# Performance work log

Hardware: AMD Instinct MI355X
Metric: run time of the kernel (lower is better)

## Reference

```python
import jax, jax.numpy as jnp
import numpy as np

B, T, D, H = 2, 2048, 1024, 16
DK = D // H  # 64


def setup_inputs() -> dict:
    key = jax.random.key(0)
    ks = jax.random.split(key, 13)
    s = 1.0 / np.sqrt(D)
    return {
        "x": jax.random.normal(ks[0], (B, T, D), jnp.float32),
        "Wq_w": jax.random.normal(ks[1], (D, D), jnp.float32) * s,
        "Wq_b": jax.random.normal(ks[2], (D,), jnp.float32) * 0.01,
        "Wk_w": jax.random.normal(ks[3], (D, D), jnp.float32) * s,
        "Wk_b": jax.random.normal(ks[4], (D,), jnp.float32) * 0.01,
        "Wv_w": jax.random.normal(ks[5], (D, D), jnp.float32) * s,
        "Wv_b": jax.random.normal(ks[6], (D,), jnp.float32) * 0.01,
        "Wo_w": jax.random.normal(ks[7], (D, D), jnp.float32) * s,
        "Wo_b": jax.random.normal(ks[8], (D,), jnp.float32) * 0.01,
        "qr": jax.random.normal(ks[9], (B, H, T, DK), jnp.float32),
        "qi": jax.random.normal(ks[10], (B, H, T, DK), jnp.float32),
        "kr": jax.random.normal(ks[11], (B, H, T, DK), jnp.float32),
        "ki": jax.random.normal(ks[12], (B, H, T, DK), jnp.float32),
    }


def _heads(y):
    # [B,T,D] -> [B,H,T,DK]
    return y.reshape(B, T, H, DK).transpose(0, 2, 1, 3)


def reference(x, Wq_w, Wq_b, Wk_w, Wk_b, Wv_w, Wv_b, Wo_w, Wo_b, qr, qi, kr, ki):
    Q = _heads(x @ Wq_w.T + Wq_b)
    K = _heads(x @ Wk_w.T + Wk_b)
    V = _heads(x @ Wv_w.T + Wv_b)
    # quantum noise: sin(atan2(imag, real))
    Q = Q + jnp.sin(jnp.arctan2(qi, qr))
    K = K + jnp.sin(jnp.arctan2(ki, kr))
    # Recursive fractal attention collapses: branches are identical and
    # deterministic, so (A1+A2)/2 == depth-0 attention at every level.
    scores = jnp.einsum("bhtd,bhsd->bhts", Q, K) / np.sqrt(DK).astype(np.float32)
    weights = jax.nn.softmax(scores, axis=-1)
    attn = jnp.einsum("bhts,bhsd->bhtd", weights, V)  # [B,H,T,DK]
    out = attn.transpose(0, 2, 1, 3).reshape(B, T, D)
    return out @ Wo_w.T + Wo_b
```

## Files before the change

### kernel.cpp

```cpp
#include <hip/hip_runtime.h>
#include <hip/hip_fp16.h>
#include <stdint.h>

typedef _Float16 half_t;
typedef _Float16 hf2 __attribute__((ext_vector_type(2)));
typedef _Float16 hf4 __attribute__((ext_vector_type(4)));
typedef _Float16 hf8 __attribute__((ext_vector_type(8)));
typedef float f32x16 __attribute__((ext_vector_type(16)));
typedef unsigned uint2_t __attribute__((ext_vector_type(2)));

#define LOG2E 1.4426950408889634f
#define SM_M 16.0f

__device__ __forceinline__ void gload16(const void* g, void* l) {
  __builtin_amdgcn_global_load_lds(
      (const __attribute__((address_space(1))) unsigned int*)g,
      (__attribute__((address_space(3))) unsigned int*)l, 16, 0, 0);
}

__device__ __forceinline__ unsigned packrtz(float a, float b) {
  auto h = __builtin_amdgcn_cvt_pkrtz(a, b);
  union { decltype(h) h2; unsigned u; } c;
  c.h2 = h;
  return c.u;
}

__global__ __launch_bounds__(256) void cvt_kernel(
    const float* __restrict__ x, const float* __restrict__ wq,
    const float* __restrict__ wk, const float* __restrict__ wv,
    const float* __restrict__ wo, half_t* __restrict__ xh,
    half_t* __restrict__ wh) {
  long e = ((long)blockIdx.x * 256 + threadIdx.x) * 16;
  const float* src;
  half_t* dst;
  if (e < 4194304L) {
    src = x + e;
    dst = xh + e;
  } else {
    long j = e - 4194304L;
    int w = (int)(j >> 20);
    long off = j & 1048575L;
    src = (w == 0 ? wq : w == 1 ? wk : w == 2 ? wv : wo) + off;
    dst = wh + ((long)w << 20) + off;
  }
  const float4* s4 = (const float4*)src;
  float4 f0 = s4[0], f1 = s4[1], f2 = s4[2], f3 = s4[3];
  hf8 o0 = {(half_t)f0.x, (half_t)f0.y, (half_t)f0.z, (half_t)f0.w,
            (half_t)f1.x, (half_t)f1.y, (half_t)f1.z, (half_t)f1.w};
  hf8 o1 = {(half_t)f2.x, (half_t)f2.y, (half_t)f2.z, (half_t)f2.w,
            (half_t)f3.x, (half_t)f3.y, (half_t)f3.z, (half_t)f3.w};
  *(hf8*)dst = o0;
  *(hf8*)(dst + 8) = o1;
}

__device__ __forceinline__ void gemm_core(const half_t* __restrict__ A,
                                          const half_t* __restrict__ Bt,
                                          int m0, int n0, half_t* ldsA,
                                          half_t* ldsB, f32x16 acc[2][2]) {
  const int tid = threadIdx.x;
  const int wid = tid >> 6;
  const int lane = tid & 63;
  const int l31 = lane & 31;
  const int hh = lane >> 5;
  const int wm = wid >> 1, wn = wid & 1;

#pragma unroll
  for (int mt = 0; mt < 2; mt++)
#pragma unroll
    for (int nt = 0; nt < 2; nt++)
#pragma unroll
      for (int i = 0; i < 16; i++) acc[mt][nt][i] = 0.f;

  for (int kt = 0; kt < 16; ++kt) {
#pragma unroll
    for (int i = 0; i < 4; i++) {
      int c = i * 256 + tid;
      int row = c >> 3;
      int c16 = (c & 7) ^ (row & 7);
      gload16(A + (long)(m0 + row) * 1024 + kt * 64 + c16 * 8,
              ldsA + i * 2048 + wid * 512);
      gload16(Bt + (long)(n0 + row) * 1024 + kt * 64 + c16 * 8,
              ldsB + i * 2048 + wid * 512);
    }
    __syncthreads();
#pragma unroll
    for (int kc = 0; kc < 4; kc++) {
      hf8 af[2], bf[2];
#pragma unroll
      for (int mt = 0; mt < 2; mt++) {
        int row = wm * 64 + mt * 32 + l31;
        af[mt] = *(const hf8*)((const char*)ldsA + row * 128 +
                               ((kc * 32 + hh * 16) ^ ((row & 7) << 4)));
      }
#pragma unroll
      for (int nt = 0; nt < 2; nt++) {
        int row = wn * 64 + nt * 32 + l31;
        bf[nt] = *(const hf8*)((const char*)ldsB + row * 128 +
                               ((kc * 32 + hh * 16) ^ ((row & 7) << 4)));
      }
#pragma unroll
      for (int mt = 0; mt < 2; mt++)
#pragma unroll
        for (int nt = 0; nt < 2; nt++)
          acc[mt][nt] = __builtin_amdgcn_mfma_f32_32x32x16_f16(
              af[mt], bf[nt], acc[mt][nt], 0, 0, 0);
    }
    __syncthreads();
  }
}

__global__ __launch_bounds__(256, 2) void proj_kernel(
    const half_t* __restrict__ xh, const half_t* __restrict__ wh,
    const float* __restrict__ bq, const float* __restrict__ bk,
    const float* __restrict__ bv, const float* __restrict__ qr,
    const float* __restrict__ qi, const float* __restrict__ kr,
    const float* __restrict__ ki, half_t* __restrict__ Qh,
    half_t* __restrict__ Kh, half_t* __restrict__ Vth) {
  __shared__ __align__(16) half_t ldsA[128 * 64];
  __shared__ __align__(16) half_t ldsB[128 * 64];
  const int z = blockIdx.z;
  const half_t* Bt = wh + (size_t)z * 1048576;
  const int m0 = blockIdx.x * 128, n0 = blockIdx.y * 128;
  f32x16 acc[2][2];
  gemm_core(xh, Bt, m0, n0, ldsA, ldsB, acc);

  const int tid = threadIdx.x;
  const int wid = tid >> 6;
  const int lane = tid & 63;
  const int l31 = lane & 31;
  const int hh = lane >> 5;
  const int wm = wid >> 1, wn = wid & 1;
  const float* bias = (z == 0) ? bq : (z == 1) ? bk : bv;
  const float* nr = (z == 0) ? qr : kr;
  const float* ni = (z == 0) ? qi : ki;
  const float scale = (z == 0) ? (0.125f * LOG2E) : 1.0f;

#pragma unroll
  for (int nt = 0; nt < 2; nt++) {
    const int n = n0 + wn * 64 + nt * 32 + l31;
    const float bsv = bias[n];
    const int hd = n >> 6, d = n & 63;
#pragma unroll
    for (int mt = 0; mt < 2; mt++) {
      const int mbase = m0 + wm * 64 + mt * 32;
      if (z == 2) {
#pragma unroll
        for (int g = 0; g < 4; g++) {
          const int m = mbase + 8 * g + 4 * hh;
          const int bb = m >> 11, tt = m & 2047;
          hf4 pk;
#pragma unroll
          for (int i2 = 0; i2 < 4; i2++)
            pk[i2] = (half_t)(acc[mt][nt][4 * g + i2] + bsv);
          *(hf4*)(Vth + (((size_t)(bb * 16 + hd) * 64 + d) * 2048 + tt)) = pk;
        }
      } else {
        half_t* dstp = (z == 0) ? Qh : Kh;
#pragma unroll
        for (int r = 0; r < 16; r++) {
          const int m = mbase + (r & 3) + 8 * (r >> 2) + 4 * hh;
          const int bb = m >> 11, tt = m & 2047;
          const size_t idx = ((size_t)(bb * 16 + hd) * 2048 + tt) * 64 + d;
          float v = acc[mt][nt][r] + bsv;
          const float a_ = nr[idx], b_ = ni[idx];
          v += b_ * rsqrtf(a_ * a_ + b_ * b_);
          dstp[idx] = (half_t)(v * scale);
        }
      }
    }
  }
}

__global__ __launch_bounds__(512, 4) void attn_kernel(
    const half_t* __restrict__ Qh, const half_t* __restrict__ Kh,
    const half_t* __restrict__ Vth, half_t* __restrict__ ah) {
  __shared__ __align__(16) char smem[65536];
  const int tid = threadIdx.x, wid = tid >> 6, lane = tid & 63;
  const int l31 = lane & 31, hh = lane >> 5;
  const int qw = wid & 3, g = wid >> 2;
  const int bh = blockIdx.y;
  const int b = bh >> 4, hd = bh & 15;
  const int t = blockIdx.x * 128 + qw * 32 + l31;

  half_t* Kl = (half_t*)(smem + g * 32768);
  half_t* Vl = Kl + 8192;

  const half_t* qrow = Qh + ((size_t)bh * 2048 + t) * 64;
  hf8 qf[4];
#pragma unroll
  for (int kc = 0; kc < 4; kc++) qf[kc] = *(const hf8*)(qrow + kc * 16 + hh * 8);

  f32x16 ot[2];
#pragma unroll
  for (int dt = 0; dt < 2; dt++)
#pragma unroll
    for (int i = 0; i < 16; i++) ot[dt][i] = 0.f;
  float lrun = 0.f;

  const half_t* Kb = Kh + (size_t)bh * 2048 * 64;
  const half_t* Vb = Vth + (size_t)bh * 64 * 2048;
  const int kvbase = g * 1024;

  {
    const int kv0 = kvbase;
#pragma unroll
    for (int i = 0; i < 2; i++) {
      int c = i * 256 + qw * 64 + lane;
      int row = c >> 3, c16 = (c & 7) ^ (row & 7);
      gload16(Kb + (size_t)(kv0 + row) * 64 + c16 * 8, Kl + i * 2048 + qw * 512);
      gload16(Vb + (size_t)row * 2048 + kv0 + c16 * 8, Vl + i * 2048 + qw * 512);
    }
  }
  __syncthreads();

  for (int tile = 0; tile < 16; ++tile) {
    const int cur = tile & 1;
    if (tile < 15) {
      const int kv0 = kvbase + (tile + 1) * 64;
      half_t* Kd = Kl + (cur ^ 1) * 4096;
      half_t* Vd = Vl + (cur ^ 1) * 4096;
#pragma unroll
      for (int i = 0; i < 2; i++) {
        int c = i * 256 + qw * 64 + lane;
        int row = c >> 3, c16 = (c & 7) ^ (row & 7);
        gload16(Kb + (size_t)(kv0 + row) * 64 + c16 * 8, Kd + i * 2048 + qw * 512);
        gload16(Vb + (size_t)row * 2048 + kv0 + c16 * 8, Vd + i * 2048 + qw * 512);
      }
    }
    const char* Kc = (const char*)(Kl + cur * 4096);
    const char* Vc = (const char*)(Vl + cur * 4096);

    f32x16 s[2];
#pragma unroll
    for (int kt = 0; kt < 2; kt++)
#pragma unroll
      for (int i = 0; i < 16; i++) s[kt][i] = 0.f;
#pragma unroll
    for (int kt = 0; kt < 2; kt++)
#pragma unroll
      for (int kc = 0; kc < 4; kc++) {
        int row = kt * 32 + l31;
        hf8 kf = *(const hf8*)(Kc + row * 128 +
                               ((kc * 32 + hh * 16) ^ ((row & 7) << 4)));
        s[kt] = __builtin_amdgcn_mfma_f32_32x32x16_f16(kf, qf[kc], s[kt], 0, 0, 0);
      }

    float psum = 0.f;
#pragma unroll
    for (int kt = 0; kt < 2; kt++)
#pragma unroll
      for (int r = 0; r < 16; r++) {
        float p = exp2f(s[kt][r] - SM_M);
        s[kt][r] = p;
        psum += p;
      }
    psum += __shfl_xor(psum, 32, 64);
    lrun += psum;

#pragma unroll
    for (int kt = 0; kt < 2; kt++) {
      unsigned pw[8];
#pragma unroll
      for (int j = 0; j < 8; j++) pw[j] = packrtz(s[kt][2 * j], s[kt][2 * j + 1]);
#pragma unroll
      for (int sub = 0; sub < 2; sub++) {
        const int kc = kt * 2 + sub;
        unsigned a0 = pw[sub * 4 + 0], a1 = pw[sub * 4 + 1];
        unsigned a2 = pw[sub * 4 + 2], a3 = pw[sub * 4 + 3];
        union { unsigned u[4]; hf8 v; } pu;
#if __has_builtin(__builtin_amdgcn_permlane32_swap)
        uint2_t r02 = __builtin_amdgcn_permlane32_swap(a0, a2, false, false);
        uint2_t r13 = __builtin_amdgcn_permlane32_swap(a1, a3, false, false);
        pu.u[0] = r02[0];
        pu.u[1] = r13[0];
        pu.u[2] = r02[1];
        pu.u[3] = r13[1];
#else
        unsigned x0 = __shfl_xor(a0, 32, 64), x1 = __shfl_xor(a1, 32, 64);
        unsigned x2 = __shfl_xor(a2, 32, 64), x3 = __shfl_xor(a3, 32, 64);
        pu.u[0] = hh ? x2 : a0;
        pu.u[1] = hh ? x3 : a1;
        pu.u[2] = hh ? a2 : x0;
        pu.u[3] = hh ? a3 : x1;
#endif
#pragma unroll
        for (int dt = 0; dt < 2; dt++) {
          int row = dt * 32 + l31;
          hf8 vf = *(const hf8*)(Vc + row * 128 +
                                 ((kc * 32 + hh * 16) ^ ((row & 7) << 4)));
          ot[dt] = __builtin_amdgcn_mfma_f32_32x32x16_f16(vf, pu.v, ot[dt], 0, 0, 0);
        }
      }
    }
    __syncthreads();
  }

  float* cb = (float*)smem;
  float* lb = (float*)(smem + 32768);
  if (g == 1) {
#pragma unroll
    for (int dt = 0; dt < 2; dt++)
#pragma unroll
      for (int i = 0; i < 16; i++)
        cb[((qw * 2 + dt) * 16 + i) * 64 + lane] = ot[dt][i];
    lb[qw * 64 + lane] = lrun;
  }
  __syncthreads();
  if (g == 0) {
#pragma unroll
    for (int dt = 0; dt < 2; dt++)
#pragma unroll
      for (int i = 0; i < 16; i++)
        ot[dt][i] += cb[((qw * 2 + dt) * 16 + i) * 64 + lane];
    const float inv = 1.0f / (lrun + lb[qw * 64 + lane]);
    const size_t obase = ((size_t)b * 2048 + t) * 1024 + hd * 64;
#pragma unroll
    for (int dt = 0; dt < 2; dt++)
#pragma unroll
      for (int gg = 0; gg < 4; gg++) {
        hf4 pk;
#pragma unroll
        for (int i2 = 0; i2 < 4; i2++)
          pk[i2] = (half_t)(ot[dt][4 * gg + i2] * inv);
        *(hf4*)(ah + obase + dt * 32 + 8 * gg + 4 * hh) = pk;
      }
  }
}

__global__ __launch_bounds__(256, 2) void outproj_kernel(
    const half_t* __restrict__ ah, const half_t* __restrict__ woh,
    const float* __restrict__ bo, float* __restrict__ out) {
  __shared__ __align__(16) half_t ldsA[128 * 64];
  __shared__ __align__(16) half_t ldsB[128 * 64];
  const int m0 = blockIdx.x * 128, n0 = blockIdx.y * 128;
  f32x16 acc[2][2];
  gemm_core(ah, woh, m0, n0, ldsA, ldsB, acc);
  const int tid = threadIdx.x, wid = tid >> 6, lane = tid & 63;
  const int l31 = lane & 31, hh = lane >> 5;
  const int wm = wid >> 1, wn = wid & 1;
#pragma unroll
  for (int nt = 0; nt < 2; nt++) {
    const int n = n0 + wn * 64 + nt * 32 + l31;
    const float bsv = bo[n];
#pragma unroll
    for (int mt = 0; mt < 2; mt++) {
      const int mbase = m0 + wm * 64 + mt * 32;
#pragma unroll
      for (int r = 0; r < 16; r++) {
        const int m = mbase + (r & 3) + 8 * (r >> 2) + 4 * hh;
        out[(size_t)m * 1024 + n] = acc[mt][nt][r] + bsv;
      }
    }
  }
}

extern "C" void kernel_launch(void* const* d_in, const int* in_sizes, int n_in,
                              void* d_out, int out_size, void* d_ws,
                              size_t ws_size, hipStream_t stream) {
  const float* x = (const float*)d_in[0];
  const float* Wq = (const float*)d_in[1];
  const float* bq = (const float*)d_in[2];
  const float* Wk = (const float*)d_in[3];
  const float* bk = (const float*)d_in[4];
  const float* Wv = (const float*)d_in[5];
  const float* bv = (const float*)d_in[6];
  const float* Wo = (const float*)d_in[7];
  const float* bo = (const float*)d_in[8];
  const float* qr = (const float*)d_in[9];
  const float* qi = (const float*)d_in[10];
  const float* kr = (const float*)d_in[11];
  const float* ki = (const float*)d_in[12];
  float* out = (float*)d_out;

  char* ws = (char*)d_ws;
  half_t* xh = (half_t*)(ws);
  half_t* wh = (half_t*)(ws + 8388608);
  half_t* Qh = (half_t*)(ws + 16777216);
  half_t* Kh = (half_t*)(ws + 25165824);
  half_t* Vth = (half_t*)(ws + 33554432);
  half_t* ah = (half_t*)(ws + 41943040);

  cvt_kernel<<<dim3(2048), dim3(256), 0, stream>>>(x, Wq, Wk, Wv, Wo, xh, wh);
  proj_kernel<<<dim3(32, 8, 3), dim3(256), 0, stream>>>(
      xh, wh, bq, bk, bv, qr, qi, kr, ki, Qh, Kh, Vth);
  attn_kernel<<<dim3(16, 32), dim3(512), 0, stream>>>(Qh, Kh, Vth, ah);
  outproj_kernel<<<dim3(32, 8), dim3(256), 0, stream>>>(ah, wh + 3 * 1048576, bo,
                                                        out);
}
```

Baseline: 124.5 us.

## Double-buffer GEMM LDS tiles and streamline attention inner loop

The projection GEMMs switch from a single LDS buffer with load-then-sync each k-step to a two-buffer ping-pong, prefetching the next k-tile while the current one is consumed, which halves the barriers. Global and LDS addresses are precomputed once and advanced by pointer increments. The attention loop is unrolled by two with precomputed LDS pointers and folds the softmax offset into the MFMA accumulator init. It also adds s_setprio around the MFMA blocks and defers the cross-half row-sum shuffle to the end. The cost is doubled LDS per GEMM block (64KB), which may reduce occupancy.

After: 185.9 us. 1.49x slower.

```diff
diff --git a/kernel.cpp b/kernel.cpp
--- a/kernel.cpp
+++ b/kernel.cpp
@@ -3,7 +3,6 @@
 #include <stdint.h>
 
 typedef _Float16 half_t;
-typedef _Float16 hf2 __attribute__((ext_vector_type(2)));
 typedef _Float16 hf4 __attribute__((ext_vector_type(4)));
 typedef _Float16 hf8 __attribute__((ext_vector_type(8)));
 typedef float f32x16 __attribute__((ext_vector_type(16)));
@@ -53,6 +52,40 @@
   *(hf8*)(dst + 8) = o1;
 }
 
+__device__ __forceinline__ void gemm_tile(bool stage, int cur,
+                                          const half_t* const gA[4],
+                                          const half_t* const gB[4],
+                                          half_t* ldsA, half_t* ldsB, int wid,
+                                          const char* const ab[4],
+                                          const char* const bb[4],
+                                          f32x16 acc[2][2]) {
+  if (stage) {
+#pragma unroll
+    for (int i = 0; i < 4; i++) {
+      gload16(gA[i], ldsA + (cur ^ 1) * 8192 + i * 2048 + wid * 512);
+      gload16(gB[i], ldsB + (cur ^ 1) * 8192 + i * 2048 + wid * 512);
+    }
+  }
+  const int cb = cur * 16384;
+#pragma unroll
+  for (int kc = 0; kc < 4; kc++) {
+    hf8 af[2], bf[2];
+#pragma unroll
+    for (int mt = 0; mt < 2; mt++)
+      af[mt] = *(const hf8*)(ab[kc] + cb + mt * 4096);
+#pragma unroll
+    for (int nt = 0; nt < 2; nt++)
+      bf[nt] = *(const hf8*)(bb[kc] + cb + nt * 4096);
+#pragma unroll
+    for (int mt = 0; mt < 2; mt++)
+#pragma unroll
+      for (int nt = 0; nt < 2; nt++)
+        acc[mt][nt] = __builtin_amdgcn_mfma_f32_32x32x16_f16(
+            af[mt], bf[nt], acc[mt][nt], 0, 0, 0);
+  }
+  __syncthreads();
+}
+
 __device__ __forceinline__ void gemm_core(const half_t* __restrict__ A,
                                           const half_t* __restrict__ Bt,
                                           int m0, int n0, half_t* ldsA,
@@ -71,41 +104,40 @@
 #pragma unroll
       for (int i = 0; i < 16; i++) acc[mt][nt][i] = 0.f;
 
-  for (int kt = 0; kt < 16; ++kt) {
-#pragma unroll
-    for (int i = 0; i < 4; i++) {
-      int c = i * 256 + tid;
-      int row = c >> 3;
-      int c16 = (c & 7) ^ (row & 7);
-      gload16(A + (long)(m0 + row) * 1024 + kt * 64 + c16 * 8,
-              ldsA + i * 2048 + wid * 512);
-      gload16(Bt + (long)(n0 + row) * 1024 + kt * 64 + c16 * 8,
-              ldsB + i * 2048 + wid * 512);
-    }
-    __syncthreads();
-#pragma unroll
-    for (int kc = 0; kc < 4; kc++) {
-      hf8 af[2], bf[2];
-#pragma unroll
-      for (int mt = 0; mt < 2; mt++) {
-        int row = wm * 64 + mt * 32 + l31;
-        af[mt] = *(const hf8*)((const char*)ldsA + row * 128 +
-                               ((kc * 32 + hh * 16) ^ ((row & 7) << 4)));
-      }
-#pragma unroll
-      for (int nt = 0; nt < 2; nt++) {
-        int row = wn * 64 + nt * 32 + l31;
-        bf[nt] = *(const hf8*)((const char*)ldsB + row * 128 +
-                               ((kc * 32 + hh * 16) ^ ((row & 7) << 4)));
-      }
-#pragma unroll
-      for (int mt = 0; mt < 2; mt++)
-#pragma unroll
-        for (int nt = 0; nt < 2; nt++)
-          acc[mt][nt] = __builtin_amdgcn_mfma_f32_32x32x16_f16(
-              af[mt], bf[nt], acc[mt][nt], 0, 0, 0);
-    }
-    __syncthreads();
+  const half_t* gA[4];
+  const half_t* gB[4];
+#pragma unroll
+  for (int i = 0; i < 4; i++) {
+    int c = i * 256 + tid;
+    int row = c >> 3;
+    int c16 = (c & 7) ^ (row & 7);
+    gA[i] = A + (long)(m0 + row) * 1024 + c16 * 8;
+    gB[i] = Bt + (long)(n0 + row) * 1024 + c16 * 8;
+  }
+  const char* ab[4];
+  const char* bb[4];
+#pragma unroll
+  for (int kc = 0; kc < 4; kc++) {
+    int swz = (kc * 32 + hh * 16) ^ ((l31 & 7) << 4);
+    ab[kc] = (const char*)ldsA + wm * 8192 + l31 * 128 + swz;
+    bb[kc] = (const char*)ldsB + wn * 8192 + l31 * 128 + swz;
+  }
+#pragma unroll
+  for (int i = 0; i < 4; i++) {
+    gload16(gA[i], ldsA + i * 2048 + wid * 512);
+    gload16(gB[i], ldsB + i * 2048 + wid * 512);
+    gA[i] += 64;
+    gB[i] += 64;
+  }
+  __syncthreads();
+
+  for (int kp = 0; kp < 8; ++kp) {
+    gemm_tile(true, 0, gA, gB, ldsA, ldsB, wid, ab, bb, acc);
+#pragma unroll
+    for (int i = 0; i < 4; i++) { gA[i] += 64; gB[i] += 64; }
+    gemm_tile(kp < 7, 1, gA, gB, ldsA, ldsB, wid, ab, bb, acc);
+#pragma unroll
+    for (int i = 0; i < 4; i++) { gA[i] += 64; gB[i] += 64; }
   }
 }
 
@@ -116,8 +148,8 @@
     const float* __restrict__ qi, const float* __restrict__ kr,
     const float* __restrict__ ki, half_t* __restrict__ Qh,
     half_t* __restrict__ Kh, half_t* __restrict__ Vth) {
-  __shared__ __align__(16) half_t ldsA[128 * 64];
-  __shared__ __align__(16) half_t ldsB[128 * 64];
+  __shared__ __align__(16) half_t ldsA[2 * 8192];
+  __shared__ __align__(16) half_t ldsB[2 * 8192];
   const int z = blockIdx.z;
   const half_t* Bt = wh + (size_t)z * 1048576;
   const int m0 = blockIdx.x * 128, n0 = blockIdx.y * 128;
@@ -171,6 +203,80 @@
   }
 }
 
+__device__ __forceinline__ void attn_tile(
+    bool stage, int cur, const half_t* gk0, const half_t* gk1,
+    const half_t* gv0, const half_t* gv1, half_t* KV, int qw,
+    const char* const kb[4], const hf8 qf[4], const f32x16& mneg,
+    f32x16 ot[2], float& psAcc) {
+  if (stage) {
+    half_t* Kd = KV + (cur ^ 1) * 4096;
+    gload16(gk0, Kd + qw * 512);
+    gload16(gk1, Kd + 2048 + qw * 512);
+    half_t* Vd = KV + 8192 + (cur ^ 1) * 4096;
+    gload16(gv0, Vd + qw * 512);
+    gload16(gv1, Vd + 2048 + qw * 512);
+  }
+  const int cb = cur * 8192;
+  f32x16 s[2];
+  __builtin_amdgcn_s_setprio(1);
+#pragma unroll
+  for (int kt = 0; kt < 2; kt++) {
+    s[kt] = __builtin_amdgcn_mfma_f32_32x32x16_f16(
+        *(const hf8*)(kb[0] + cb + kt * 4096), qf[0], mneg, 0, 0, 0);
+#pragma unroll
+    for (int kc = 1; kc < 4; kc++)
+      s[kt] = __builtin_amdgcn_mfma_f32_32x32x16_f16(
+          *(const hf8*)(kb[kc] + cb + kt * 4096), qf[kc], s[kt], 0, 0, 0);
+  }
+  __builtin_amdgcn_s_setprio(0);
+
+#pragma unroll
+  for (int kt = 0; kt < 2; kt++) {
+    unsigned pw[8];
+    float pa = 0.f, pb = 0.f;
+#pragma unroll
+    for (int j = 0; j < 8; j++) {
+      float p0 = exp2f(s[kt][2 * j]);
+      float p1 = exp2f(s[kt][2 * j + 1]);
+      pa += p0;
+      pb += p1;
+      pw[j] = packrtz(p0, p1);
+    }
+    psAcc += pa + pb;
+#pragma unroll
+    for (int sub = 0; sub < 2; sub++) {
+      const int kc = kt * 2 + sub;
+      unsigned a0 = pw[sub * 4 + 0], a1 = pw[sub * 4 + 1];
+      unsigned a2 = pw[sub * 4 + 2], a3 = pw[sub * 4 + 3];
+      union { unsigned u[4]; hf8 v; } pu;
+#if __has_builtin(__builtin_amdgcn_permlane32_swap)
+      uint2_t r02 = __builtin_amdgcn_permlane32_swap(a0, a2, false, false);
+      uint2_t r13 = __builtin_amdgcn_permlane32_swap(a1, a3, false, false);
+      pu.u[0] = r02[0];
+      pu.u[1] = r13[0];
+      pu.u[2] = r02[1];
+      pu.u[3] = r13[1];
+#else
+      const int hh_ = (threadIdx.x & 63) >> 5;
+      unsigned x0 = __shfl_xor(a0, 32, 64), x1 = __shfl_xor(a1, 32, 64);
+      unsigned x2 = __shfl_xor(a2, 32, 64), x3 = __shfl_xor(a3, 32, 64);
+      pu.u[0] = hh_ ? x2 : a0;
+      pu.u[1] = hh_ ? x3 : a1;
+      pu.u[2] = hh_ ? a2 : x0;
+      pu.u[3] = hh_ ? a3 : x1;
+#endif
+      __builtin_amdgcn_s_setprio(1);
+#pragma unroll
+      for (int dt = 0; dt < 2; dt++) {
+        hf8 vf = *(const hf8*)(kb[kc] + 16384 + cb + dt * 4096);
+        ot[dt] = __builtin_amdgcn_mfma_f32_32x32x16_f16(vf, pu.v, ot[dt], 0, 0, 0);
+      }
+      __builtin_amdgcn_s_setprio(0);
+    }
+  }
+  __syncthreads();
+}
+
 __global__ __launch_bounds__(512, 4) void attn_kernel(
     const half_t* __restrict__ Qh, const half_t* __restrict__ Kh,
     const half_t* __restrict__ Vth, half_t* __restrict__ ah) {
@@ -182,8 +288,7 @@
   const int b = bh >> 4, hd = bh & 15;
   const int t = blockIdx.x * 128 + qw * 32 + l31;
 
-  half_t* Kl = (half_t*)(smem + g * 32768);
-  half_t* Vl = Kl + 8192;
+  half_t* KV = (half_t*)(smem + g * 32768);
 
   const half_t* qrow = Qh + ((size_t)bh * 2048 + t) * 64;
   hf8 qf[4];
@@ -195,105 +300,50 @@
   for (int dt = 0; dt < 2; dt++)
 #pragma unroll
     for (int i = 0; i < 16; i++) ot[dt][i] = 0.f;
-  float lrun = 0.f;
+  f32x16 mneg;
+#pragma unroll
+  for (int i = 0; i < 16; i++) mneg[i] = -SM_M;
+  float psAcc = 0.f;
 
   const half_t* Kb = Kh + (size_t)bh * 2048 * 64;
   const half_t* Vb = Vth + (size_t)bh * 64 * 2048;
   const int kvbase = g * 1024;
 
-  {
-    const int kv0 = kvbase;
-#pragma unroll
-    for (int i = 0; i < 2; i++) {
-      int c = i * 256 + qw * 64 + lane;
-      int row = c >> 3, c16 = (c & 7) ^ (row & 7);
-      gload16(Kb + (size_t)(kv0 + row) * 64 + c16 * 8, Kl + i * 2048 + qw * 512);
-      gload16(Vb + (size_t)row * 2048 + kv0 + c16 * 8, Vl + i * 2048 + qw * 512);
-    }
-  }
+  const char* kbp[4];
+#pragma unroll
+  for (int kc = 0; kc < 4; kc++)
+    kbp[kc] = (const char*)KV + l31 * 128 +
+              ((kc * 32 + hh * 16) ^ ((l31 & 7) << 4));
+
+  const half_t* gk[2];
+  const half_t* gv[2];
+#pragma unroll
+  for (int i = 0; i < 2; i++) {
+    int c = i * 256 + qw * 64 + lane;
+    int row = c >> 3, c16 = (c & 7) ^ (row & 7);
+    gk[i] = Kb + (size_t)(kvbase + row) * 64 + c16 * 8;
+    gv[i] = Vb + (size_t)row * 2048 + kvbase + c16 * 8;
+  }
+  gload16(gk[0], KV + qw * 512);
+  gload16(gk[1], KV + 2048 + qw * 512);
+  gload16(gv[0], KV + 8192 + qw * 512);
+  gload16(gv[1], KV + 8192 + 2048 + qw * 512);
+#pragma unroll
+  for (int i = 0; i < 2; i++) { gk[i] += 4096; gv[i] += 64; }
   __syncthreads();
 
-  for (int tile = 0; tile < 16; ++tile) {
-    const int cur = tile & 1;
-    if (tile < 15) {
-      const int kv0 = kvbase + (tile + 1) * 64;
-      half_t* Kd = Kl + (cur ^ 1) * 4096;
-      half_t* Vd = Vl + (cur ^ 1) * 4096;
-#pragma unroll
-      for (int i = 0; i < 2; i++) {
-        int c = i * 256 + qw * 64 + lane;
-        int row = c >> 3, c16 = (c & 7) ^ (row & 7);
-        gload16(Kb + (size_t)(kv0 + row) * 64 + c16 * 8, Kd + i * 2048 + qw * 512);
-        gload16(Vb + (size_t)row * 2048 + kv0 + c16 * 8, Vd + i * 2048 + qw * 512);
-      }
-    }
-    const char* Kc = (const char*)(Kl + cur * 4096);
-    const char* Vc = (const char*)(Vl + cur * 4096);
-
-    f32x16 s[2];
-#pragma unroll
-    for (int kt = 0; kt < 2; kt++)
-#pragma unroll
-      for (int i = 0; i < 16; i++) s[kt][i] = 0.f;
-#pragma unroll
-    for (int kt = 0; kt < 2; kt++)
-#pragma unroll
-      for (int kc = 0; kc < 4; kc++) {
-        int row = kt * 32 + l31;
-        hf8 kf = *(const hf8*)(Kc + row * 128 +
-                               ((kc * 32 + hh * 16) ^ ((row & 7) << 4)));
-        s[kt] = __builtin_amdgcn_mfma_f32_32x32x16_f16(kf, qf[kc], s[kt], 0, 0, 0);
-      }
-
-    float psum = 0.f;
-#pragma unroll
-    for (int kt = 0; kt < 2; kt++)
-#pragma unroll
-      for (int r = 0; r < 16; r++) {
-        float p = exp2f(s[kt][r] - SM_M);
-        s[kt][r] = p;
-        psum += p;
-      }
-    psum += __shfl_xor(psum, 32, 64);
-    lrun += psum;
-
-#pragma unroll
-    for (int kt = 0; kt < 2; kt++) {
-      unsigned pw[8];
-#pragma unroll
-      for (int j = 0; j < 8; j++) pw[j] = packrtz(s[kt][2 * j], s[kt][2 * j + 1]);
-#pragma unroll
-      for (int sub = 0; sub < 2; sub++) {
-        const int kc = kt * 2 + sub;
-        unsigned a0 = pw[sub * 4 + 0], a1 = pw[sub * 4 + 1];
-        unsigned a2 = pw[sub * 4 + 2], a3 = pw[sub * 4 + 3];
-        union { unsigned u[4]; hf8 v; } pu;
-#if __has_builtin(__builtin_amdgcn_permlane32_swap)
-        uint2_t r02 = __builtin_amdgcn_permlane32_swap(a0, a2, false, false);
-        uint2_t r13 = __builtin_amdgcn_permlane32_swap(a1, a3, false, false);
-        pu.u[0] = r02[0];
-        pu.u[1] = r13[0];
-        pu.u[2] = r02[1];
-        pu.u[3] = r13[1];
-#else
-        unsigned x0 = __shfl_xor(a0, 32, 64), x1 = __shfl_xor(a1, 32, 64);
-        unsigned x2 = __shfl_xor(a2, 32, 64), x3 = __shfl_xor(a3, 32, 64);
-        pu.u[0] = hh ? x2 : a0;
-        pu.u[1] = hh ? x3 : a1;
-        pu.u[2] = hh ? a2 : x0;
-        pu.u[3] = hh ? a3 : x1;
-#endif
-#pragma unroll
-        for (int dt = 0; dt < 2; dt++) {
-          int row = dt * 32 + l31;
-          hf8 vf = *(const hf8*)(Vc + row * 128 +
-                                 ((kc * 32 + hh * 16) ^ ((row & 7) << 4)));
-          ot[dt] = __builtin_amdgcn_mfma_f32_32x32x16_f16(vf, pu.v, ot[dt], 0, 0, 0);
-        }
-      }
-    }
-    __syncthreads();
-  }
+  for (int tp = 0; tp < 8; ++tp) {
+    attn_tile(true, 0, gk[0], gk[1], gv[0], gv[1], KV, qw, kbp, qf, mneg, ot,
+              psAcc);
+#pragma unroll
+    for (int i = 0; i < 2; i++) { gk[i] += 4096; gv[i] += 64; }
+    attn_tile(tp < 7, 1, gk[0], gk[1], gv[0], gv[1], KV, qw, kbp, qf, mneg, ot,
+              psAcc);
+#pragma unroll
+    for (int i = 0; i < 2; i++) { gk[i] += 4096; gv[i] += 64; }
+  }
+
+  const float lrun = psAcc + __shfl_xor(psAcc, 32, 64);
 
   float* cb = (float*)smem;
   float* lb = (float*)(smem + 32768);
@@ -330,8 +380,8 @@
 __global__ __launch_bounds__(256, 2) void outproj_kernel(
     const half_t* __restrict__ ah, const half_t* __restrict__ woh,
     const float* __restrict__ bo, float* __restrict__ out) {
-  __shared__ __align__(16) half_t ldsA[128 * 64];
-  __shared__ __align__(16) half_t ldsB[128 * 64];
+  __shared__ __align__(16) half_t ldsA[2 * 8192];
+  __shared__ __align__(16) half_t ldsB[2 * 8192];
   const int m0 = blockIdx.x * 128, n0 = blockIdx.y * 128;
   f32x16 acc[2][2];
   gemm_core(ah, woh, m0, n0, ldsA, ldsB, acc);
```
